# Kernel tuning notes

Hardware: AMD Instinct MI355X
Metric: run time of the kernel (lower is better)

The kernel has to match this reference:

```python
import jax, jax.numpy as jnp
import numpy as np

DIM = 2048
N_HEADS = 16
N_KV_HEADS = 8
HEAD_DIM = DIM // N_HEADS  # 128
N_REP = N_HEADS // N_KV_HEADS  # 2
B, L = 2, 2048
ROPE_THETA = 10000.0


def make_freqs_cis(L, head_dim, theta):
    inv = 1.0 / (theta ** (np.arange(0, head_dim, 2, dtype=np.float32) / head_dim))
    t = np.arange(L, dtype=np.float32)
    ang = np.outer(t, inv)  # [L, head_dim//2]
    return jnp.asarray(np.stack([np.cos(ang), np.sin(ang)], axis=-1))  # [L, hd//2, 2]


def setup_inputs() -> dict:
    key = jax.random.key(0)
    ks = jax.random.split(key, 5)
    s = 1.0 / np.sqrt(DIM)
    return {
        "x": jax.random.normal(ks[0], (B, L, DIM), dtype=jnp.float32),
        "freqs_cis": make_freqs_cis(L, HEAD_DIM, ROPE_THETA),
        "wq": jax.random.normal(ks[1], (DIM, N_HEADS * HEAD_DIM), dtype=jnp.float32) * s,
        "wk": jax.random.normal(ks[2], (DIM, N_KV_HEADS * HEAD_DIM), dtype=jnp.float32) * s,
        "wv": jax.random.normal(ks[3], (DIM, N_KV_HEADS * HEAD_DIM), dtype=jnp.float32) * s,
        "wo": jax.random.normal(ks[4], (N_HEADS * HEAD_DIM, DIM), dtype=jnp.float32) * s,
    }


def apply_rotary(x, freqs_cis):
    # x: [B, L, H, D]; freqs_cis: [L, D//2, 2] (cos, sin)
    xr = x.reshape(*x.shape[:-1], -1, 2)  # [B,L,H,D//2,2]
    cos = freqs_cis[None, :, None, :, 0]
    sin = freqs_cis[None, :, None, :, 1]
    out_r = xr[..., 0] * cos - xr[..., 1] * sin
    out_i = xr[..., 0] * sin + xr[..., 1] * cos
    return jnp.stack([out_r, out_i], axis=-1).reshape(x.shape).astype(x.dtype)


def reference(x, freqs_cis, wq, wk, wv, wo):
    Bx, Lx, _ = x.shape
    xq = (x @ wq).reshape(Bx, Lx, N_HEADS, HEAD_DIM)
    xk = (x @ wk).reshape(Bx, Lx, N_KV_HEADS, HEAD_DIM)
    xv = (x @ wv).reshape(Bx, Lx, N_KV_HEADS, HEAD_DIM)
    xq = apply_rotary(xq, freqs_cis)
    xk = apply_rotary(xk, freqs_cis)
    # repeat kv heads (GQA) then put heads first: [B, H, L, D]
    keys = jnp.repeat(xk, N_REP, axis=2).transpose(0, 2, 1, 3)
    values = jnp.repeat(xv, N_REP, axis=2).transpose(0, 2, 1, 3)
    xq = xq.transpose(0, 2, 1, 3)
    scores = jnp.einsum("bhqd,bhkd->bhqk", xq, keys) / jnp.sqrt(
        jnp.asarray(HEAD_DIM, dtype=xq.dtype))
    causal = jnp.tril(jnp.ones((Lx, Lx), dtype=bool))
    scores = jnp.where(causal[None, None], scores, -jnp.inf)
    probs = jax.nn.softmax(scores.astype(jnp.float32), axis=-1).astype(xq.dtype)
    out = jnp.einsum("bhqk,bhkd->bhqd", probs, values)
    out = out.transpose(0, 2, 1, 3).reshape(Bx, Lx, -1)
    return out @ wo
```

## Files before the change

### kernel.cpp

```cpp
#include <hip/hip_runtime.h>
#include <math.h>

typedef unsigned short u16;
typedef unsigned int   u32;
typedef u16   u16x8 __attribute__((ext_vector_type(8)));
typedef u16   u16x4 __attribute__((ext_vector_type(4)));
typedef u16   u16x2 __attribute__((ext_vector_type(2)));
typedef __bf16 bf16x8 __attribute__((ext_vector_type(8)));
typedef float  f32x4 __attribute__((ext_vector_type(4)));

__device__ __forceinline__ u16 f2b(float f) {
    union { float f; u32 u; } v; v.f = f;
    u32 u = v.u;
    return (u16)((u + 0x7FFFu + ((u >> 16) & 1u)) >> 16);
}

__device__ __forceinline__ void glds16(const void* g, void* l) {
    __builtin_amdgcn_global_load_lds(
        (__attribute__((address_space(1))) void*)(void*)g,
        (__attribute__((address_space(3))) void*)l, 16, 0, 0);
}

__global__ __launch_bounds__(256) void convert_f32_bf16(
    const float* __restrict__ src, u16* __restrict__ dst)
{
    const size_t i = ((size_t)blockIdx.x * 256 + threadIdx.x) * 8;
    f32x4 a = *(const f32x4*)&src[i];
    f32x4 b = *(const f32x4*)&src[i + 4];
    u16x8 o;
    #pragma unroll
    for (int j = 0; j < 4; ++j) { o[j] = f2b(a[j]); o[4 + j] = f2b(b[j]); }
    *(u16x8*)&dst[i] = o;
}

__global__ __launch_bounds__(256) void transpose_f32_bf16(
    const float* __restrict__ src, u16* __restrict__ dst, int R, int C)
{
    __shared__ u16 tile[64 * 72];
    const int t = threadIdx.x;
    const int r0 = blockIdx.y * 64, c0 = blockIdx.x * 64;
    #pragma unroll
    for (int i = 0; i < 2; ++i) {
        int idx = i * 256 + t;
        int r = idx >> 3, c8 = (idx & 7) * 8;
        const float* sp = &src[(size_t)(r0 + r) * C + c0 + c8];
        f32x4 a = *(const f32x4*)sp;
        f32x4 b = *(const f32x4*)(sp + 4);
        u16x8 v;
        #pragma unroll
        for (int j = 0; j < 4; ++j) { v[j] = f2b(a[j]); v[4 + j] = f2b(b[j]); }
        *(u16x8*)&tile[r * 72 + c8] = v;
    }
    __syncthreads();
    #pragma unroll
    for (int i = 0; i < 2; ++i) {
        int idx = i * 256 + t;
        int orow = idx >> 3, oc8 = (idx & 7) * 8;
        u16x8 w;
        #pragma unroll
        for (int j = 0; j < 8; ++j) w[j] = tile[(oc8 + j) * 72 + orow];
        *(u16x8*)&dst[(size_t)(c0 + orow) * R + r0 + oc8] = w;
    }
}

template <int MODE>
__global__ __launch_bounds__(256) void gemm_bt(
    const u16* __restrict__ A, const u16* __restrict__ Bt,
    u16* __restrict__ D0, u16* __restrict__ D1, u16* __restrict__ D2,
    float* __restrict__ Fout, const float* __restrict__ fc)
{
    __shared__ u16 Alds[128 * 32];
    __shared__ u16 Blds[128 * 32];
    const int t = threadIdx.x;
    const int wid = t >> 6, lane = t & 63;
    const int l15 = lane & 15, qd = lane >> 4;
    const int row0 = blockIdx.y * 128, col0 = blockIdx.x * 128;
    const int wm = (wid >> 1) * 64, wn = (wid & 1) * 64;

    const int sm = lane >> 2;
    const int sk = (lane & 3) * 8;
    const int c0 = wid * 2;
    const u16* Ag0 = A  + (size_t)(row0 + c0 * 16 + sm) * 2048 + sk;
    const u16* Ag1 = A  + (size_t)(row0 + (c0 + 1) * 16 + sm) * 2048 + sk;
    const u16* Bg0 = Bt + (size_t)(col0 + c0 * 16 + sm) * 2048 + sk;
    const u16* Bg1 = Bt + (size_t)(col0 + (c0 + 1) * 16 + sm) * 2048 + sk;
    u16* Al0 = Alds + c0 * 512; u16* Al1 = Alds + (c0 + 1) * 512;
    u16* Bl0 = Blds + c0 * 512; u16* Bl1 = Blds + (c0 + 1) * 512;

    f32x4 acc[4][4] = {};

    for (int k0 = 0; k0 < 2048; k0 += 32) {
        glds16(Ag0 + k0, Al0);
        glds16(Ag1 + k0, Al1);
        glds16(Bg0 + k0, Bl0);
        glds16(Bg1 + k0, Bl1);
        __syncthreads();
        bf16x8 af[4], bfr[4];
        #pragma unroll
        for (int mt = 0; mt < 4; ++mt)
            af[mt] = *(const bf16x8*)&Alds[(wm + mt * 16 + l15) * 32 + qd * 8];
        #pragma unroll
        for (int nt = 0; nt < 4; ++nt)
            bfr[nt] = *(const bf16x8*)&Blds[(wn + nt * 16 + l15) * 32 + qd * 8];
        __builtin_amdgcn_s_setprio(1);
        #pragma unroll
        for (int mt = 0; mt < 4; ++mt)
            #pragma unroll
            for (int nt = 0; nt < 4; ++nt)
                acc[mt][nt] = __builtin_amdgcn_mfma_f32_16x16x32_bf16(
                    af[mt], bfr[nt], acc[mt][nt], 0, 0, 0);
        __builtin_amdgcn_s_setprio(0);
        __syncthreads();
    }

    #pragma unroll
    for (int mt = 0; mt < 4; ++mt)
        #pragma unroll
        for (int nt = 0; nt < 4; ++nt) {
            const int gcol = col0 + wn + nt * 16 + l15;
            const int grow0 = row0 + wm + mt * 16 + qd * 4;
            if (MODE == 1) {
                #pragma unroll
                for (int r = 0; r < 4; ++r)
                    Fout[(size_t)(grow0 + r) * 2048 + gcol] = acc[mt][nt][r];
            } else if (gcol >= 3072) {
                const int vcol = gcol - 3072;
                const int vrow = vcol + (grow0 >> 11) * 1024;
                u16x4 v;
                #pragma unroll
                for (int r = 0; r < 4; ++r) v[r] = f2b(acc[mt][nt][r]);
                *(u16x4*)&D2[(size_t)vrow * 2048 + (grow0 & 2047)] = v;
            } else {
                const int p2 = gcol & 126;
                #pragma unroll
                for (int r = 0; r < 4; ++r) {
                    const int l = (grow0 + r) & 2047;
                    const float c = fc[l * 128 + p2];
                    const float s = fc[l * 128 + p2 + 1];
                    const float own = acc[mt][nt][r];
                    const float oth = __shfl_xor(own, 1);
                    const float rot = (l15 & 1) ? (oth * s + own * c)
                                                : (own * c - oth * s);
                    const u16 v = f2b(rot);
                    if (gcol < 2048)
                        D0[(size_t)(grow0 + r) * 2048 + gcol] = v;
                    else
                        D1[(size_t)(grow0 + r) * 1024 + (gcol - 2048)] = v;
                }
            }
        }
}

__global__ __launch_bounds__(256, 2) void attn_kernel(
    const u16* __restrict__ Q, const u16* __restrict__ K,
    const u16* __restrict__ Vt, u16* __restrict__ AO)
{
    __shared__ u16 SM[32768];
    const int t = threadIdx.x;
    const int w = t >> 6, lane = t & 63;
    const int l15 = lane & 15, qd = lane >> 4;
    const int b = blockIdx.x >> 3, kvh = blockIdx.x & 7;
    const int y = (int)blockIdx.y;
    const int qt = (y < 16) ? (31 - y) : (y - 16);
    const int h = kvh * 2 + (w >> 1);
    const float SCL = 0.08838834764831845f * 1.4426950408889634f;

    u16* K0 = SM;
    u16* K1 = SM + 8192;
    u16* VB = SM + 16384;
    u16* PW = SM + 24576 + w * 2048;

    bf16x8 qf[2][4];
    #pragma unroll
    for (int mt = 0; mt < 2; ++mt) {
        const size_t grow = (size_t)b * 2048 + qt * 64 + (w & 1) * 32 + mt * 16 + l15;
        const u16* qp = Q + grow * 2048 + h * 128 + qd * 8;
        #pragma unroll
        for (int ks = 0; ks < 4; ++ks)
            qf[mt][ks] = *(const bf16x8*)(qp + ks * 32);
    }
    f32x4 Oa[2][8] = {};
    f32x4 Ls[2] = {};
    bf16x8 onesv;
    #pragma unroll
    for (int j = 0; j < 8; ++j) onesv[j] = (__bf16)1.0f;

    const u16* Kbase = K  + (size_t)b * 2048 * 1024 + kvh * 128;
    const u16* Vbase = Vt + (size_t)(b * 8 + kvh) * 128 * 2048;

    #pragma unroll
    for (int j = 0; j < 4; ++j) {
        const int f = w * 4 + j;
        glds16(Kbase + (size_t)((f >> 2) * 16 + l15) * 1024 + ((f & 3) * 4 + qd) * 8,
               K0 + f * 512);
    }
    __syncthreads();

    for (int kt = 0; kt <= qt; ++kt) {
        u16* Kc = (kt & 1) ? K1 : K0;
        u16* Kn = (kt & 1) ? K0 : K1;
        if (kt < qt) {
            #pragma unroll
            for (int j = 0; j < 4; ++j) {
                const int f = w * 4 + j;
                glds16(Kbase + (size_t)((kt + 1) * 64 + (f >> 2) * 16 + l15) * 1024
                             + ((f & 3) * 4 + qd) * 8,
                       Kn + f * 512);
            }
        }
        #pragma unroll
        for (int j = 0; j < 4; ++j) {
            const int f = w * 4 + j;
            glds16(Vbase + (size_t)((f >> 1) * 16 + l15) * 2048 + kt * 64
                         + ((f & 1) * 4 + qd) * 8,
                   VB + f * 512);
        }

        f32x4 S[2][4] = {};
        #pragma unroll
        for (int ks = 0; ks < 4; ++ks) {
            bf16x8 bk[4];
            #pragma unroll
            for (int nt = 0; nt < 4; ++nt)
                bk[nt] = *(const bf16x8*)&Kc[(nt * 4 + ks) * 512 + lane * 8];
            __builtin_amdgcn_s_setprio(1);
            #pragma unroll
            for (int mt = 0; mt < 2; ++mt)
                #pragma unroll
                for (int nt = 0; nt < 4; ++nt)
                    S[mt][nt] = __builtin_amdgcn_mfma_f32_16x16x32_bf16(
                        qf[mt][ks], bk[nt], S[mt][nt], 0, 0, 0);
            __builtin_amdgcn_s_setprio(0);
        }
        if (kt == qt) {
            #pragma unroll
            for (int mt = 0; mt < 2; ++mt)
                #pragma unroll
                for (int r = 0; r < 4; ++r) {
                    const int qg = (w & 1) * 32 + mt * 16 + qd * 4 + r;
                    #pragma unroll
                    for (int nt = 0; nt < 4; ++nt)
                        if (nt * 16 + l15 > qg) S[mt][nt][r] = -__builtin_inff();
                }
        }
        #pragma unroll
        for (int mt = 0; mt < 2; ++mt)
            #pragma unroll
            for (int nt = 0; nt < 4; ++nt)
                #pragma unroll
                for (int r = 0; r < 4; ++r) {
                    const float p = exp2f(S[mt][nt][r] * SCL - 12.0f);
                    PW[(mt * 2 + (nt >> 1)) * 512 + ((nt * 2 + (l15 >> 3)) & 3) * 128
                       + (qd * 4 + r) * 8 + (l15 & 7)] = f2b(p);
                }

        __syncthreads();

        #pragma unroll
        for (int ks = 0; ks < 2; ++ks) {
            bf16x8 pa[2], vb[8];
            #pragma unroll
            for (int mt = 0; mt < 2; ++mt)
                pa[mt] = *(const bf16x8*)&PW[(mt * 2 + ks) * 512 + lane * 8];
            #pragma unroll
            for (int nt = 0; nt < 8; ++nt)
                vb[nt] = *(const bf16x8*)&VB[(nt * 2 + ks) * 512 + lane * 8];
            __builtin_amdgcn_s_setprio(1);
            #pragma unroll
            for (int mt = 0; mt < 2; ++mt) {
                Ls[mt] = __builtin_amdgcn_mfma_f32_16x16x32_bf16(
                    pa[mt], onesv, Ls[mt], 0, 0, 0);
                #pragma unroll
                for (int nt = 0; nt < 8; ++nt)
                    Oa[mt][nt] = __builtin_amdgcn_mfma_f32_16x16x32_bf16(
                        pa[mt], vb[nt], Oa[mt][nt], 0, 0, 0);
            }
            __builtin_amdgcn_s_setprio(0);
        }
        __syncthreads();
    }

    u16* OL = SM;
    #pragma unroll
    for (int mt = 0; mt < 2; ++mt)
        #pragma unroll
        for (int r = 0; r < 4; ++r) {
            const float inv = 1.f / Ls[mt][r];
            const int qr = (w & 1) * 32 + mt * 16 + qd * 4 + r;
            #pragma unroll
            for (int nt = 0; nt < 8; ++nt)
                OL[qr * 256 + (w >> 1) * 128 + nt * 16 + l15] = f2b(Oa[mt][nt][r] * inv);
        }
    __syncthreads();
    #pragma unroll
    for (int i = 0; i < 8; ++i) {
        const int c = i * 256 + t;
        const int row = c >> 5, ch = c & 31;
        u16x8 v = *(const u16x8*)&OL[row * 256 + ch * 8];
        *(u16x8*)&AO[((size_t)b * 2048 + qt * 64 + row) * 2048 + kvh * 256 + ch * 8] = v;
    }
}

extern "C" void kernel_launch(void* const* d_in, const int* in_sizes, int n_in,
                              void* d_out, int out_size, void* d_ws, size_t ws_size,
                              hipStream_t stream)
{
    (void)in_sizes; (void)n_in; (void)out_size; (void)ws_size;
    const float* x  = (const float*)d_in[0];
    const float* fc = (const float*)d_in[1];
    const float* wq = (const float*)d_in[2];
    const float* wk = (const float*)d_in[3];
    const float* wv = (const float*)d_in[4];
    const float* wo = (const float*)d_in[5];
    float* out = (float*)d_out;
    char* ws = (char*)d_ws;

    u16* Qb  = (u16*)(ws);
    u16* Kb  = (u16*)(ws + 16777216);
    u16* Vt  = (u16*)(ws + 25165824);
    u16* Xb  = (u16*)(ws + 33554432);
    u16* AO  = (u16*)(ws + 33554432);
    u16* WT  = (u16*)(ws + 50331648);
    u16* WOT = (u16*)(ws + 67108864);

    convert_f32_bf16<<<4096, 256, 0, stream>>>(x, Xb);
    transpose_f32_bf16<<<dim3(32, 32), 256, 0, stream>>>(wq, WT, 2048, 2048);
    transpose_f32_bf16<<<dim3(16, 32), 256, 0, stream>>>(wk, WT + 2048 * 2048, 2048, 1024);
    transpose_f32_bf16<<<dim3(16, 32), 256, 0, stream>>>(wv, WT + 3072 * 2048, 2048, 1024);
    transpose_f32_bf16<<<dim3(32, 32), 256, 0, stream>>>(wo, WOT, 2048, 2048);

    gemm_bt<0><<<dim3(32, 32), 256, 0, stream>>>(Xb, WT, Qb, Kb, Vt, nullptr, fc);

    attn_kernel<<<dim3(16, 32), 256, 0, stream>>>(Qb, Kb, Vt, AO);

    gemm_bt<1><<<dim3(16, 32), 256, 0, stream>>>(AO, WOT, nullptr, nullptr, nullptr, out, nullptr);
}
```

Before: 266.7 us.

## Triple-buffer GEMM LDS tiles with async global-to-LDS prefetch two stages ahead

```diff
diff --git a/kernel.cpp b/kernel.cpp
--- a/kernel.cpp
+++ b/kernel.cpp
@@ -69,8 +69,8 @@
     u16* __restrict__ D0, u16* __restrict__ D1, u16* __restrict__ D2,
     float* __restrict__ Fout, const float* __restrict__ fc)
 {
-    __shared__ u16 Alds[128 * 32];
-    __shared__ u16 Blds[128 * 32];
+    __shared__ u16 SA[3 * 4096];
+    __shared__ u16 SB[3 * 4096];
     const int t = threadIdx.x;
     const int wid = t >> 6, lane = t & 63;
     const int l15 = lane & 15, qd = lane >> 4;
@@ -84,33 +84,46 @@
     const u16* Ag1 = A  + (size_t)(row0 + (c0 + 1) * 16 + sm) * 2048 + sk;
     const u16* Bg0 = Bt + (size_t)(col0 + c0 * 16 + sm) * 2048 + sk;
     const u16* Bg1 = Bt + (size_t)(col0 + (c0 + 1) * 16 + sm) * 2048 + sk;
-    u16* Al0 = Alds + c0 * 512; u16* Al1 = Alds + (c0 + 1) * 512;
-    u16* Bl0 = Blds + c0 * 512; u16* Bl1 = Blds + (c0 + 1) * 512;
+    const int lo0 = c0 * 512, lo1 = (c0 + 1) * 512;
+
+    u16 *pa0 = SA, *pa1 = SA + 4096, *pa2 = SA + 8192;
+    u16 *pb0 = SB, *pb1 = SB + 4096, *pb2 = SB + 8192;
 
     f32x4 acc[4][4] = {};
 
-    for (int k0 = 0; k0 < 2048; k0 += 32) {
-        glds16(Ag0 + k0, Al0);
-        glds16(Ag1 + k0, Al1);
-        glds16(Bg0 + k0, Bl0);
-        glds16(Bg1 + k0, Bl1);
-        __syncthreads();
+    glds16(Ag0, pa0 + lo0); glds16(Ag1, pa0 + lo1);
+    glds16(Bg0, pb0 + lo0); glds16(Bg1, pb0 + lo1);
+    glds16(Ag0 + 32, pa1 + lo0); glds16(Ag1 + 32, pa1 + lo1);
+    glds16(Bg0 + 32, pb1 + lo0); glds16(Bg1 + 32, pb1 + lo1);
+    asm volatile("s_waitcnt vmcnt(4)" ::: "memory");
+    __builtin_amdgcn_s_barrier();
+
+    for (int kt = 0; kt < 64; ++kt) {
+        if (kt < 62) {
+            const int ko = (kt + 2) * 32;
+            glds16(Ag0 + ko, pa2 + lo0); glds16(Ag1 + ko, pa2 + lo1);
+            glds16(Bg0 + ko, pb2 + lo0); glds16(Bg1 + ko, pb2 + lo1);
+        }
         bf16x8 af[4], bfr[4];
         #pragma unroll
         for (int mt = 0; mt < 4; ++mt)
-            af[mt] = *(const bf16x8*)&Alds[(wm + mt * 16 + l15) * 32 + qd * 8];
+            af[mt] = *(const bf16x8*)&pa0[(wm + mt * 16 + l15) * 32 + qd * 8];
         #pragma unroll
         for (int nt = 0; nt < 4; ++nt)
-            bfr[nt] = *(const bf16x8*)&Blds[(wn + nt * 16 + l15) * 32 + qd * 8];
-        __builtin_amdgcn_s_setprio(1);
+            bfr[nt] = *(const bf16x8*)&pb0[(wn + nt * 16 + l15) * 32 + qd * 8];
         #pragma unroll
         for (int mt = 0; mt < 4; ++mt)
             #pragma unroll
             for (int nt = 0; nt < 4; ++nt)
                 acc[mt][nt] = __builtin_amdgcn_mfma_f32_16x16x32_bf16(
                     af[mt], bfr[nt], acc[mt][nt], 0, 0, 0);
-        __builtin_amdgcn_s_setprio(0);
-        __syncthreads();
+        if (kt < 62)
+            asm volatile("s_waitcnt vmcnt(4)" ::: "memory");
+        else if (kt == 62)
+            asm volatile("s_waitcnt vmcnt(0)" ::: "memory");
+        if (kt < 63) __builtin_amdgcn_s_barrier();
+        u16* ta = pa0; pa0 = pa1; pa1 = pa2; pa2 = ta;
+        u16* tb = pb0; pb0 = pb1; pb1 = pb2; pb2 = tb;
     }
 
     #pragma unroll
```

Result: no change. 270.8 us (+1.5%).
